# Performance work log

Measured on AMD Instinct MI355X. Metric: run time of the kernel, lower is better.

Reference implementation:

```python
import jax, jax.numpy as jnp
import numpy as np

D_MODEL = 512
D_INNER = 2 * D_MODEL          # Mamba expand=2
D_STATE = 16                   # Mamba default d_state
D_CONV = 4                     # Mamba default d_conv
DT_RANK = D_MODEL // 16        # ceil(512/16) = 32
B, L = 2, 2048


def setup_inputs() -> dict:
    key = jax.random.key(0)
    ks = jax.random.split(key, 12)
    s = 0.02
    return {
        "query": jax.random.normal(ks[0], (B, L, D_MODEL), jnp.float32),
        "value": jax.random.normal(ks[1], (B, L, D_MODEL), jnp.float32),
        "diff_ts": jax.random.normal(ks[2], (B, D_MODEL), jnp.float32),
        # AdaLN modulation: SiLU -> Linear(D, 2D) (random instead of zero-init to exercise math)
        "ada_w": jax.random.normal(ks[3], (2 * D_MODEL, D_MODEL), jnp.float32) * s,
        "ada_b": jax.random.normal(ks[4], (2 * D_MODEL,), jnp.float32) * s,
        # Mamba params
        "in_proj_w": jax.random.normal(ks[5], (2 * D_INNER, D_MODEL), jnp.float32) * s,
        "conv_w": jax.random.normal(ks[6], (D_INNER, D_CONV), jnp.float32) * 0.1,
        "conv_b": jax.random.normal(ks[7], (D_INNER,), jnp.float32) * 0.1,
        "x_proj_w": jax.random.normal(ks[8], (DT_RANK + 2 * D_STATE, D_INNER), jnp.float32) * s,
        "dt_proj_w": jax.random.normal(ks[9], (D_INNER, DT_RANK), jnp.float32) * 0.1,
        "dt_proj_b": jax.random.normal(ks[10], (D_INNER,), jnp.float32) * 0.1,
        "A_log": jnp.broadcast_to(jnp.log(jnp.arange(1, D_STATE + 1, dtype=jnp.float32)), (D_INNER, D_STATE)) * jnp.ones((D_INNER, 1), jnp.float32),
        "D_param": jnp.ones((D_INNER,), jnp.float32),
        "out_proj_w": jax.random.normal(ks[11], (D_MODEL, D_INNER), jnp.float32) * s,
        "ln_g": jnp.ones((D_MODEL,), jnp.float32),
        "ln_b": jnp.zeros((D_MODEL,), jnp.float32),
    }


def reference(query, value, diff_ts, ada_w, ada_b, in_proj_w, conv_w, conv_b,
              x_proj_w, dt_proj_w, dt_proj_b, A_log, D_param, out_proj_w, ln_g, ln_b):
    silu = jax.nn.silu
    # ---- AdaLN modulation of query ----
    m = silu(diff_ts) @ ada_w.T + ada_b            # (B, 2D)
    scale, shift = jnp.split(m, 2, axis=-1)        # (B, D) each
    x = query * (1.0 + scale[:, None, :]) + shift[:, None, :]

    # ---- Mamba block ----
    xz = x @ in_proj_w.T                           # (B, L, 2*d_inner)
    xm, z = jnp.split(xz, 2, axis=-1)
    # causal depthwise conv1d (kernel D_CONV)
    xp = jnp.pad(xm, ((0, 0), (D_CONV - 1, 0), (0, 0)))
    Lq = xm.shape[1]
    xc = sum(xp[:, k:k + Lq, :] * conv_w[:, k] for k in range(D_CONV)) + conv_b
    xc = silu(xc)                                  # (B, L, d_inner)

    xdb = xc @ x_proj_w.T                          # (B, L, dt_rank + 2*N)
    dt = xdb[..., :DT_RANK]
    Bm = xdb[..., DT_RANK:DT_RANK + D_STATE]       # (B, L, N)
    Cm = xdb[..., DT_RANK + D_STATE:]              # (B, L, N)
    delta = jax.nn.softplus(dt @ dt_proj_w.T + dt_proj_b)  # (B, L, d_inner)
    A = -jnp.exp(A_log)                            # (d_inner, N)

    # ---- selective scan: h_t = exp(dt*A) h_{t-1} + dt*B_t*x_t ; y_t = C_t . h_t ----
    def step(h, inp):
        d_t, x_t, B_t, C_t = inp                   # (B,d), (B,d), (B,N), (B,N)
        dA = jnp.exp(d_t[..., None] * A)           # (B, d, N)
        h = dA * h + (d_t * x_t)[..., None] * B_t[:, None, :]
        y = jnp.einsum('bdn,bn->bd', h, C_t)
        return h, y

    seq = (delta.transpose(1, 0, 2), xc.transpose(1, 0, 2),
           Bm.transpose(1, 0, 2), Cm.transpose(1, 0, 2))
    h0 = jnp.zeros((query.shape[0], D_INNER, D_STATE), delta.dtype)
    _, ys = jax.lax.scan(step, h0, seq)            # (L, B, d_inner)

    y = ys.transpose(1, 0, 2) + xc * D_param
    y = y * silu(z)
    attn = y @ out_proj_w.T                        # (B, L, D)

    # ---- residual (dropout p=0) + LayerNorm ----
    out = query + attn
    mu = out.mean(-1, keepdims=True)
    var = out.var(-1, keepdims=True)
    return (out - mu) / jnp.sqrt(var + 1e-5) * ln_g + ln_b
```

## Files before the change

### kernel.cpp

```cpp
#include <hip/hip_runtime.h>
#include <hip/hip_bf16.h>

#define D_MODEL 512
#define D_INNER 1024
#define D_STATE 16
#define DT_RANK 32
#define BB 2
#define LL 2048
#define RR (BB*LL)
#define NC 128
#define CS 16

typedef __attribute__((ext_vector_type(8))) short short8;
typedef __attribute__((ext_vector_type(4))) short short4v;
typedef __attribute__((ext_vector_type(4))) float f32x4;

static __device__ __forceinline__ short f2bf(float f) {
  union { __hip_bfloat16 h; short s; } u;
  u.h = __float2bfloat16(f);
  return u.s;
}

__global__ void k_ada_cvtw(const float* __restrict__ diff,
                           const float* __restrict__ aw,
                           const float* __restrict__ ab,
                           float* __restrict__ m,
                           const float* __restrict__ inw,
                           const float* __restrict__ outw,
                           short* __restrict__ inwb,
                           short* __restrict__ outwb) {
  const int bx = blockIdx.x;
  const int t = threadIdx.x;
  if (bx < 8) {
    __shared__ float sd[D_MODEL];
    const int b = bx >> 2;
    const int jb = bx & 3;
    for (int k = t; k < D_MODEL; k += 256) {
      float v = diff[b*D_MODEL + k];
      sd[k] = v / (1.f + __expf(-v));
    }
    __syncthreads();
    const int j = jb*256 + t;
    const float4* wr = reinterpret_cast<const float4*>(aw + (size_t)j*D_MODEL);
    float acc = ab[j];
    #pragma unroll 4
    for (int k4 = 0; k4 < D_MODEL/4; ++k4) {
      float4 wv = wr[k4];
      acc += sd[4*k4]*wv.x + sd[4*k4+1]*wv.y + sd[4*k4+2]*wv.z + sd[4*k4+3]*wv.w;
    }
    m[b*(2*D_MODEL) + j] = acc;
  } else {
    const int N1 = 2048*512, N2 = 512*1024;
    const int idx = ((bx - 8)*256 + t)*4;
    if (idx < N1) {
      float4 v = *reinterpret_cast<const float4*>(inw + idx);
      short4v s = {f2bf(v.x), f2bf(v.y), f2bf(v.z), f2bf(v.w)};
      *reinterpret_cast<short4v*>(inwb + idx) = s;
    } else if (idx < N1 + N2) {
      float4 v = *reinterpret_cast<const float4*>(outw + (idx - N1));
      short4v s = {f2bf(v.x), f2bf(v.y), f2bf(v.z), f2bf(v.w)};
      *reinterpret_cast<short4v*>(outwb + (idx - N1)) = s;
    }
  }
}

__global__ void k_amod(const float* __restrict__ q,
                       const float* __restrict__ m,
                       short* __restrict__ amod) {
  const int gid = blockIdx.x*256 + threadIdx.x;
  const int idx = gid*4;
  const int r = idx >> 9, k = idx & 511;
  const float* mrow = m + (r >> 11)*(2*D_MODEL);
  float4 a = *reinterpret_cast<const float4*>(q + idx);
  float4 s = *reinterpret_cast<const float4*>(mrow + k);
  float4 h = *reinterpret_cast<const float4*>(mrow + D_MODEL + k);
  short4v o = {f2bf(a.x*(1.f+s.x)+h.x), f2bf(a.y*(1.f+s.y)+h.y),
               f2bf(a.z*(1.f+s.z)+h.z), f2bf(a.w*(1.f+s.w)+h.w)};
  *reinterpret_cast<short4v*>(amod + idx) = o;
}

__global__ void __launch_bounds__(256) k_gemm_bf16(
    const short* __restrict__ A,
    const short* __restrict__ B,
    float* __restrict__ C,
    int K, int ldc) {
  __shared__ short As[128][48];
  __shared__ short Bs[64][48];
  const int t = threadIdx.x;
  const int wave = t >> 6, lane = t & 63;
  const int quad = lane >> 4, l16 = lane & 15;
  const int row0 = blockIdx.y*128;
  const int col0 = blockIdx.x*64;
  f32x4 acc[2][4] = {};
  for (int k0 = 0; k0 < K; k0 += 32) {
    #pragma unroll
    for (int i = 0; i < 2; ++i) {
      int e = t + i*256;
      int ar = e >> 2, ak = (e & 3)*8;
      *reinterpret_cast<short8*>(&As[ar][ak]) =
          *reinterpret_cast<const short8*>(A + (size_t)(row0+ar)*K + k0 + ak);
    }
    {
      int br = t >> 2, bk = (t & 3)*8;
      *reinterpret_cast<short8*>(&Bs[br][bk]) =
          *reinterpret_cast<const short8*>(B + (size_t)(col0+br)*K + k0 + bk);
    }
    __syncthreads();
    short8 af[2], bf[4];
    #pragma unroll
    for (int i = 0; i < 2; ++i)
      af[i] = *reinterpret_cast<const short8*>(&As[wave*32 + i*16 + l16][quad*8]);
    #pragma unroll
    for (int j = 0; j < 4; ++j)
      bf[j] = *reinterpret_cast<const short8*>(&Bs[j*16 + l16][quad*8]);
    #pragma unroll
    for (int i = 0; i < 2; ++i)
      #pragma unroll
      for (int j = 0; j < 4; ++j)
        acc[i][j] = __builtin_amdgcn_mfma_f32_16x16x32_bf16(af[i], bf[j], acc[i][j], 0, 0, 0);
    __syncthreads();
  }
  #pragma unroll
  for (int i = 0; i < 2; ++i)
    #pragma unroll
    for (int j = 0; j < 4; ++j)
      #pragma unroll
      for (int r = 0; r < 4; ++r)
        C[(size_t)(row0 + wave*32 + i*16 + quad*4 + r)*ldc + col0 + j*16 + l16] = acc[i][j][r];
}

__global__ void k_conv4(const float* __restrict__ xz,
                        const float* __restrict__ cw,
                        const float* __restrict__ cb,
                        float* __restrict__ xc) {
  const int gid = blockIdx.x*256 + threadIdx.x;
  const int d4 = (gid & 255)*4;
  const int r = gid >> 8;
  const int l = r & (LL-1);
  float4 w0 = *reinterpret_cast<const float4*>(cw + (size_t)(d4+0)*4);
  float4 w1 = *reinterpret_cast<const float4*>(cw + (size_t)(d4+1)*4);
  float4 w2 = *reinterpret_cast<const float4*>(cw + (size_t)(d4+2)*4);
  float4 w3 = *reinterpret_cast<const float4*>(cw + (size_t)(d4+3)*4);
  float4 res = *reinterpret_cast<const float4*>(cb + d4);
  #pragma unroll
  for (int k = 0; k < 4; ++k) {
    int ls = l + k - 3;
    if (ls >= 0) {
      float4 xv = *reinterpret_cast<const float4*>(xz + (size_t)(r + k - 3)*(2*D_INNER) + d4);
      float wk0 = (&w0.x)[k], wk1 = (&w1.x)[k], wk2 = (&w2.x)[k], wk3 = (&w3.x)[k];
      res.x += xv.x*wk0; res.y += xv.y*wk1; res.z += xv.z*wk2; res.w += xv.w*wk3;
    }
  }
  res.x = res.x / (1.f + __expf(-res.x));
  res.y = res.y / (1.f + __expf(-res.y));
  res.z = res.z / (1.f + __expf(-res.z));
  res.w = res.w / (1.f + __expf(-res.w));
  *reinterpret_cast<float4*>(xc + (size_t)r*D_INNER + d4) = res;
}

__global__ void k_xproj_t(const float* __restrict__ xc,
                          const float* __restrict__ xw,
                          float* __restrict__ xdb) {
  __shared__ float As[16][68];
  __shared__ float Bs[16][68];
  const int tx = threadIdx.x, ty = threadIdx.y;
  const int t = ty*16 + tx;
  const int row0 = blockIdx.y*64;
  const int kbase = blockIdx.x*128;
  float acc[4][4] = {};
  for (int k0 = kbase; k0 < kbase + 128; k0 += 16) {
    #pragma unroll
    for (int i = 0; i < 4; ++i) {
      int e = t + i*256;
      int kk = e & 15, rr = e >> 4;
      As[kk][rr] = xc[(size_t)(row0+rr)*D_INNER + k0+kk];
      Bs[kk][rr] = xw[(size_t)rr*D_INNER + k0+kk];
    }
    __syncthreads();
    #pragma unroll
    for (int kk = 0; kk < 16; ++kk) {
      float4 av = *reinterpret_cast<const float4*>(&As[kk][ty*4]);
      float4 bv = *reinterpret_cast<const float4*>(&Bs[kk][tx*4]);
      float a[4] = {av.x, av.y, av.z, av.w};
      float bq[4] = {bv.x, bv.y, bv.z, bv.w};
      #pragma unroll
      for (int i = 0; i < 4; ++i)
        #pragma unroll
        for (int j = 0; j < 4; ++j)
          acc[i][j] += a[i]*bq[j];
    }
    __syncthreads();
  }
  #pragma unroll
  for (int i = 0; i < 4; ++i)
    #pragma unroll
    for (int j = 0; j < 4; ++j)
      unsafeAtomicAdd(&xdb[(size_t)(row0+ty*4+i)*64 + tx*4 + j], acc[i][j]);
}

__global__ void __launch_bounds__(256) k_deltaf(
    const float* __restrict__ xdb,
    const float* __restrict__ dtw,
    const float* __restrict__ dtb,
    float* __restrict__ delta) {
  const int d = blockIdx.x*256 + threadIdx.x;
  const int r0 = blockIdx.y*16;
  float dwr[DT_RANK];
  const float4* dwp = reinterpret_cast<const float4*>(dtw + (size_t)d*DT_RANK);
  #pragma unroll
  for (int i = 0; i < 8; ++i) {
    float4 v = dwp[i];
    dwr[4*i]=v.x; dwr[4*i+1]=v.y; dwr[4*i+2]=v.z; dwr[4*i+3]=v.w;
  }
  const float dbv = dtb[d];
  for (int r = r0; r < r0 + 16; ++r) {
    const float4* xr = reinterpret_cast<const float4*>(xdb + (size_t)r*64);
    float acc = dbv;
    #pragma unroll
    for (int i = 0; i < 8; ++i) {
      float4 v = xr[i];
      acc += v.x*dwr[4*i] + v.y*dwr[4*i+1] + v.z*dwr[4*i+2] + v.w*dwr[4*i+3];
    }
    delta[(size_t)r*D_INNER + d] = (acc > 20.f) ? acc : __logf(1.f + __expf(acc));
  }
}


__global__ void __launch_bounds__(256) k_scan1(
    const float* __restrict__ delta,
    const float* __restrict__ xc,
    const float* __restrict__ xdb,
    float* __restrict__ rbuf,
    float* __restrict__ hstate) {
  __shared__ float sx[CS*64];
  const int tid = threadIdx.x;
  const int d = blockIdx.x*256 + tid;
  const int c = blockIdx.y;
  const int b = blockIdx.z;
  const float* xrow = xdb + ((size_t)b*LL + (size_t)c*CS)*64;
  *reinterpret_cast<float4*>(&sx[tid*4]) = *reinterpret_cast<const float4*>(xrow + tid*4);
  const size_t base = ((size_t)b*LL + (size_t)c*CS)*D_INNER + d;
  float dls[CS], xvs[CS];
  #pragma unroll
  for (int t = 0; t < CS; ++t) {
    dls[t] = delta[base + (size_t)t*D_INNER];
    xvs[t] = xc[base + (size_t)t*D_INNER];
  }
  float h[D_STATE];
  #pragma unroll
  for (int n = 0; n < D_STATE; ++n) h[n] = 0.f;
  float S = 0.f;
  __syncthreads();
  #pragma unroll
  for (int t = 0; t < CS; ++t) {
    float dlt = dls[t];
    S += dlt;
    float dx = dlt * xvs[t];
    float r = __expf(-dlt);
    float e = r;
    #pragma unroll
    for (int n = 0; n < D_STATE; ++n) {
      h[n] = e*h[n] + dx*sx[t*64 + 32 + n];
      e *= r;
    }
  }
  const size_t s0 = (((size_t)b*NC + c)*D_STATE)*D_INNER + d;
  #pragma unroll
  for (int n = 0; n < D_STATE; ++n)
    hstate[s0 + (size_t)n*D_INNER] = h[n];
  rbuf[((size_t)b*NC + c)*D_INNER + d] = __expf(-S);
}

__global__ void k_scan2(const float* __restrict__ rbuf,
                        float* __restrict__ hstate) {
  const int gid = blockIdx.x*256 + threadIdx.x;
  const int b = gid >> 14;
  const int nd = gid & 16383;
  const int n = nd >> 10;
  const int d = nd & (D_INNER-1);
  const int p = n + 1;
  float h = 0.f;
  #pragma unroll 4
  for (int c = 0; c < NC; ++c) {
    const size_t ridx = ((size_t)b*NC + c)*D_INNER + d;
    const size_t idx = (((size_t)b*NC + c)*D_STATE)*D_INNER + nd;
    float r = rbuf[ridx];
    float hl = hstate[idx];
    float r2 = r*r, r4 = r2*r2, r8 = r4*r4;
    float a = (p & 1) ? r : 1.f;
    if (p & 2)  a *= r2;
    if (p & 4)  a *= r4;
    if (p & 8)  a *= r8;
    if (p & 16) a *= r8*r8;
    hstate[idx] = h;
    h = a*h + hl;
  }
}

__global__ void __launch_bounds__(256) k_scan3(
    const float* __restrict__ delta,
    const float* __restrict__ xc,
    const float* __restrict__ xdb,
    const float* __restrict__ hstate,
    const float* __restrict__ Dp,
    const float* __restrict__ xz,
    short* __restrict__ y2b) {
  __shared__ float sx[CS*64];
  const int tid = threadIdx.x;
  const int d = blockIdx.x*256 + tid;
  const int c = blockIdx.y;
  const int b = blockIdx.z;
  const float* xrow = xdb + ((size_t)b*LL + (size_t)c*CS)*64;
  *reinterpret_cast<float4*>(&sx[tid*4]) = *reinterpret_cast<const float4*>(xrow + tid*4);
  const size_t r0 = (size_t)b*LL + (size_t)c*CS;
  const size_t base = r0*D_INNER + d;
  float dls[CS], xvs[CS], zs[CS];
  #pragma unroll
  for (int t = 0; t < CS; ++t) {
    dls[t] = delta[base + (size_t)t*D_INNER];
    xvs[t] = xc[base + (size_t)t*D_INNER];
    zs[t]  = xz[(r0 + t)*(2*D_INNER) + D_INNER + d];
  }
  float h[D_STATE];
  const size_t s0 = (((size_t)b*NC + c)*D_STATE)*D_INNER + d;
  #pragma unroll
  for (int n = 0; n < D_STATE; ++n)
    h[n] = hstate[s0 + (size_t)n*D_INNER];
  const float dp = Dp[d];
  __syncthreads();
  #pragma unroll
  for (int t = 0; t < CS; ++t) {
    float dlt = dls[t];
    float xv  = xvs[t];
    float dx = dlt * xv;
    float r = __expf(-dlt);
    float e = r;
    float acc = 0.f;
    #pragma unroll
    for (int n = 0; n < D_STATE; ++n) {
      h[n] = e*h[n] + dx*sx[t*64 + 32 + n];
      acc += h[n]*sx[t*64 + 48 + n];
      e *= r;
    }
    float z = zs[t];
    float sz = z / (1.f + __expf(-z));
    y2b[base + (size_t)t*D_INNER] = f2bf((acc + xv*dp) * sz);
  }
}

__global__ void k_ln(const float* __restrict__ attn,
                     const float* __restrict__ q,
                     const float* __restrict__ g,
                     const float* __restrict__ bb,
                     float* __restrict__ out) {
  const int r = blockIdx.x;
  const int t = threadIdx.x;
  float v0 = attn[(size_t)r*D_MODEL + t]       + q[(size_t)r*D_MODEL + t];
  float v1 = attn[(size_t)r*D_MODEL + 256 + t] + q[(size_t)r*D_MODEL + 256 + t];
  float s = v0 + v1, sq = v0*v0 + v1*v1;
  #pragma unroll
  for (int off = 32; off; off >>= 1) {
    s  += __shfl_xor(s, off);
    sq += __shfl_xor(sq, off);
  }
  __shared__ float ss[4], qq[4], stats[2];
  const int wid = t >> 6, lane = t & 63;
  if (lane == 0) { ss[wid] = s; qq[wid] = sq; }
  __syncthreads();
  if (t == 0) {
    float S = ss[0]+ss[1]+ss[2]+ss[3];
    float Q = qq[0]+qq[1]+qq[2]+qq[3];
    float mu = S * (1.f/D_MODEL);
    float var = Q * (1.f/D_MODEL) - mu*mu;
    stats[0] = mu; stats[1] = rsqrtf(var + 1e-5f);
  }
  __syncthreads();
  float mu = stats[0], rs = stats[1];
  out[(size_t)r*D_MODEL + t]       = (v0-mu)*rs*g[t]     + bb[t];
  out[(size_t)r*D_MODEL + 256 + t] = (v1-mu)*rs*g[256+t] + bb[256+t];
}

extern "C" void kernel_launch(void* const* d_in, const int* in_sizes, int n_in,
                              void* d_out, int out_size, void* d_ws, size_t ws_size,
                              hipStream_t stream) {
  (void)in_sizes; (void)n_in; (void)out_size; (void)ws_size;
  const float* q    = (const float*)d_in[0];
  const float* diff = (const float*)d_in[2];
  const float* aw   = (const float*)d_in[3];
  const float* ab   = (const float*)d_in[4];
  const float* inw  = (const float*)d_in[5];
  const float* cw   = (const float*)d_in[6];
  const float* cb   = (const float*)d_in[7];
  const float* xw   = (const float*)d_in[8];
  const float* dtw  = (const float*)d_in[9];
  const float* dtb  = (const float*)d_in[10];
  const float* Dp   = (const float*)d_in[12];
  const float* outw = (const float*)d_in[13];
  const float* lng  = (const float*)d_in[14];
  const float* lnb  = (const float*)d_in[15];
  float* out = (float*)d_out;

  float* ws = (float*)d_ws;
  float* m      = ws;
  float* xz     = ws + 2048;
  float* xc     = xz + (size_t)RR*2*D_INNER;
  float* xdb    = xc + (size_t)RR*D_INNER;
  float* rbuf   = xdb + (size_t)RR*64;
  float* hstate = rbuf + (size_t)BB*NC*D_INNER;
  float* delta  = hstate + (size_t)BB*NC*D_INNER*16;
  float* attn2  = delta + (size_t)RR*D_INNER;
  short* amod  = (short*)(attn2 + (size_t)RR*D_MODEL);
  short* inwb  = amod + (size_t)RR*D_MODEL;
  short* outwb = inwb + (size_t)2*D_INNER*D_MODEL;
  short* y2b   = outwb + (size_t)D_MODEL*D_INNER;

  k_ada_cvtw<<<8 + (2048*512 + 512*1024)/(256*4), 256, 0, stream>>>(
      diff, aw, ab, m, inw, outw, inwb, outwb);
  k_amod<<<(RR*D_MODEL)/(256*4), 256, 0, stream>>>(q, m, amod);
  k_gemm_bf16<<<dim3((2*D_INNER)/64, RR/128), 256, 0, stream>>>(amod, inwb, xz, D_MODEL, 2*D_INNER);
  k_conv4<<<(RR*D_INNER/4)/256, 256, 0, stream>>>(xz, cw, cb, xc);
  hipMemsetAsync(xdb, 0, (size_t)RR*64*sizeof(float), stream);
  k_xproj_t<<<dim3(8, RR/64), dim3(16,16), 0, stream>>>(xc, xw, xdb);
  k_deltaf<<<dim3(D_INNER/256, RR/16), 256, 0, stream>>>(xdb, dtw, dtb, delta);
  k_scan1<<<dim3(D_INNER/256, NC, BB), 256, 0, stream>>>(delta, xc, xdb, rbuf, hstate);
  k_scan2<<<(BB*D_INNER*16)/256, 256, 0, stream>>>(rbuf, hstate);
  k_scan3<<<dim3(D_INNER/256, NC, BB), 256, 0, stream>>>(delta, xc, xdb, hstate, Dp, xz, y2b);
  k_gemm_bf16<<<dim3(D_MODEL/64, RR/128), 256, 0, stream>>>(y2b, outwb, attn2, D_INNER, D_MODEL);
  k_ln<<<RR, 256, 0, stream>>>(attn2, q, lng, lnb, out);
}
```

Baseline: 281.8 us.

## Fuse delta computation into scan kernels and run x_proj as bf16 MFMA GEMM

```diff
diff --git a/kernel.cpp b/kernel.cpp
--- a/kernel.cpp
+++ b/kernel.cpp
@@ -27,8 +27,10 @@
                            float* __restrict__ m,
                            const float* __restrict__ inw,
                            const float* __restrict__ outw,
+                           const float* __restrict__ xw,
                            short* __restrict__ inwb,
-                           short* __restrict__ outwb) {
+                           short* __restrict__ outwb,
+                           short* __restrict__ xwb) {
   const int bx = blockIdx.x;
   const int t = threadIdx.x;
   if (bx < 8) {
@@ -50,7 +52,7 @@
     }
     m[b*(2*D_MODEL) + j] = acc;
   } else {
-    const int N1 = 2048*512, N2 = 512*1024;
+    const int N1 = 2048*512, N2 = 512*1024, N3 = 64*1024;
     const int idx = ((bx - 8)*256 + t)*4;
     if (idx < N1) {
       float4 v = *reinterpret_cast<const float4*>(inw + idx);
@@ -60,6 +62,10 @@
       float4 v = *reinterpret_cast<const float4*>(outw + (idx - N1));
       short4v s = {f2bf(v.x), f2bf(v.y), f2bf(v.z), f2bf(v.w)};
       *reinterpret_cast<short4v*>(outwb + (idx - N1)) = s;
+    } else if (idx < N1 + N2 + N3) {
+      float4 v = *reinterpret_cast<const float4*>(xw + (idx - N1 - N2));
+      short4v s = {f2bf(v.x), f2bf(v.y), f2bf(v.z), f2bf(v.w)};
+      *reinterpret_cast<short4v*>(xwb + (idx - N1 - N2)) = s;
     }
   }
 }
@@ -132,7 +138,8 @@
 __global__ void k_conv4(const float* __restrict__ xz,
                         const float* __restrict__ cw,
                         const float* __restrict__ cb,
-                        float* __restrict__ xc) {
+                        float* __restrict__ xc,
+                        short* __restrict__ xcb) {
   const int gid = blockIdx.x*256 + threadIdx.x;
   const int d4 = (gid & 255)*4;
   const int r = gid >> 8;
@@ -156,80 +163,16 @@
   res.z = res.z / (1.f + __expf(-res.z));
   res.w = res.w / (1.f + __expf(-res.w));
   *reinterpret_cast<float4*>(xc + (size_t)r*D_INNER + d4) = res;
-}
-
-__global__ void k_xproj_t(const float* __restrict__ xc,
-                          const float* __restrict__ xw,
-                          float* __restrict__ xdb) {
-  __shared__ float As[16][68];
-  __shared__ float Bs[16][68];
-  const int tx = threadIdx.x, ty = threadIdx.y;
-  const int t = ty*16 + tx;
-  const int row0 = blockIdx.y*64;
-  const int kbase = blockIdx.x*128;
-  float acc[4][4] = {};
-  for (int k0 = kbase; k0 < kbase + 128; k0 += 16) {
-    #pragma unroll
-    for (int i = 0; i < 4; ++i) {
-      int e = t + i*256;
-      int kk = e & 15, rr = e >> 4;
-      As[kk][rr] = xc[(size_t)(row0+rr)*D_INNER + k0+kk];
-      Bs[kk][rr] = xw[(size_t)rr*D_INNER + k0+kk];
-    }
-    __syncthreads();
-    #pragma unroll
-    for (int kk = 0; kk < 16; ++kk) {
-      float4 av = *reinterpret_cast<const float4*>(&As[kk][ty*4]);
-      float4 bv = *reinterpret_cast<const float4*>(&Bs[kk][tx*4]);
-      float a[4] = {av.x, av.y, av.z, av.w};
-      float bq[4] = {bv.x, bv.y, bv.z, bv.w};
-      #pragma unroll
-      for (int i = 0; i < 4; ++i)
-        #pragma unroll
-        for (int j = 0; j < 4; ++j)
-          acc[i][j] += a[i]*bq[j];
-    }
-    __syncthreads();
-  }
-  #pragma unroll
-  for (int i = 0; i < 4; ++i)
-    #pragma unroll
-    for (int j = 0; j < 4; ++j)
-      unsafeAtomicAdd(&xdb[(size_t)(row0+ty*4+i)*64 + tx*4 + j], acc[i][j]);
-}
-
-__global__ void __launch_bounds__(256) k_deltaf(
+  short4v rb = {f2bf(res.x), f2bf(res.y), f2bf(res.z), f2bf(res.w)};
+  *reinterpret_cast<short4v*>(xcb + (size_t)r*D_INNER + d4) = rb;
+}
+
+
+__global__ void __launch_bounds__(256) k_scan1(
+    const float* __restrict__ xc,
     const float* __restrict__ xdb,
     const float* __restrict__ dtw,
     const float* __restrict__ dtb,
-    float* __restrict__ delta) {
-  const int d = blockIdx.x*256 + threadIdx.x;
-  const int r0 = blockIdx.y*16;
-  float dwr[DT_RANK];
-  const float4* dwp = reinterpret_cast<const float4*>(dtw + (size_t)d*DT_RANK);
-  #pragma unroll
-  for (int i = 0; i < 8; ++i) {
-    float4 v = dwp[i];
-    dwr[4*i]=v.x; dwr[4*i+1]=v.y; dwr[4*i+2]=v.z; dwr[4*i+3]=v.w;
-  }
-  const float dbv = dtb[d];
-  for (int r = r0; r < r0 + 16; ++r) {
-    const float4* xr = reinterpret_cast<const float4*>(xdb + (size_t)r*64);
-    float acc = dbv;
-    #pragma unroll
-    for (int i = 0; i < 8; ++i) {
-      float4 v = xr[i];
-      acc += v.x*dwr[4*i] + v.y*dwr[4*i+1] + v.z*dwr[4*i+2] + v.w*dwr[4*i+3];
-    }
-    delta[(size_t)r*D_INNER + d] = (acc > 20.f) ? acc : __logf(1.f + __expf(acc));
-  }
-}
-
-
-__global__ void __launch_bounds__(256) k_scan1(
-    const float* __restrict__ delta,
-    const float* __restrict__ xc,
-    const float* __restrict__ xdb,
     float* __restrict__ rbuf,
     float* __restrict__ hstate) {
   __shared__ float sx[CS*64];
@@ -240,23 +183,34 @@
   const float* xrow = xdb + ((size_t)b*LL + (size_t)c*CS)*64;
   *reinterpret_cast<float4*>(&sx[tid*4]) = *reinterpret_cast<const float4*>(xrow + tid*4);
   const size_t base = ((size_t)b*LL + (size_t)c*CS)*D_INNER + d;
-  float dls[CS], xvs[CS];
+  float xvs[CS];
+  #pragma unroll
+  for (int t = 0; t < CS; ++t)
+    xvs[t] = xc[base + (size_t)t*D_INNER];
+  float dwr[DT_RANK];
+  const float4* dwp = reinterpret_cast<const float4*>(dtw + (size_t)d*DT_RANK);
+  #pragma unroll
+  for (int i = 0; i < 8; ++i) {
+    float4 v = dwp[i];
+    dwr[4*i]=v.x; dwr[4*i+1]=v.y; dwr[4*i+2]=v.z; dwr[4*i+3]=v.w;
+  }
+  const float dbv = dtb[d];
+  float h[D_STATE];
+  #pragma unroll
+  for (int n = 0; n < D_STATE; ++n) h[n] = 0.f;
+  float rtot = 1.f;
+  __syncthreads();
   #pragma unroll
   for (int t = 0; t < CS; ++t) {
-    dls[t] = delta[base + (size_t)t*D_INNER];
-    xvs[t] = xc[base + (size_t)t*D_INNER];
-  }
-  float h[D_STATE];
-  #pragma unroll
-  for (int n = 0; n < D_STATE; ++n) h[n] = 0.f;
-  float S = 0.f;
-  __syncthreads();
-  #pragma unroll
-  for (int t = 0; t < CS; ++t) {
-    float dlt = dls[t];
-    S += dlt;
+    float dacc = dbv;
+    #pragma unroll
+    for (int i = 0; i < DT_RANK; ++i)
+      dacc += sx[t*64 + i]*dwr[i];
+    float ex = __expf(dacc);
+    float dlt = (dacc > 20.f) ? dacc : __logf(1.f + ex);
+    float r = 1.f / (1.f + ex);
+    rtot *= r;
     float dx = dlt * xvs[t];
-    float r = __expf(-dlt);
     float e = r;
     #pragma unroll
     for (int n = 0; n < D_STATE; ++n) {
@@ -268,7 +222,7 @@
   #pragma unroll
   for (int n = 0; n < D_STATE; ++n)
     hstate[s0 + (size_t)n*D_INNER] = h[n];
-  rbuf[((size_t)b*NC + c)*D_INNER + d] = __expf(-S);
+  rbuf[((size_t)b*NC + c)*D_INNER + d] = rtot;
 }
 
 __global__ void k_scan2(const float* __restrict__ rbuf,
@@ -298,9 +252,10 @@
 }
 
 __global__ void __launch_bounds__(256) k_scan3(
-    const float* __restrict__ delta,
     const float* __restrict__ xc,
     const float* __restrict__ xdb,
+    const float* __restrict__ dtw,
+    const float* __restrict__ dtb,
     const float* __restrict__ hstate,
     const float* __restrict__ Dp,
     const float* __restrict__ xz,
@@ -314,13 +269,20 @@
   *reinterpret_cast<float4*>(&sx[tid*4]) = *reinterpret_cast<const float4*>(xrow + tid*4);
   const size_t r0 = (size_t)b*LL + (size_t)c*CS;
   const size_t base = r0*D_INNER + d;
-  float dls[CS], xvs[CS], zs[CS];
+  float xvs[CS], zs[CS];
   #pragma unroll
   for (int t = 0; t < CS; ++t) {
-    dls[t] = delta[base + (size_t)t*D_INNER];
     xvs[t] = xc[base + (size_t)t*D_INNER];
     zs[t]  = xz[(r0 + t)*(2*D_INNER) + D_INNER + d];
   }
+  float dwr[DT_RANK];
+  const float4* dwp = reinterpret_cast<const float4*>(dtw + (size_t)d*DT_RANK);
+  #pragma unroll
+  for (int i = 0; i < 8; ++i) {
+    float4 v = dwp[i];
+    dwr[4*i]=v.x; dwr[4*i+1]=v.y; dwr[4*i+2]=v.z; dwr[4*i+3]=v.w;
+  }
+  const float dbv = dtb[d];
   float h[D_STATE];
   const size_t s0 = (((size_t)b*NC + c)*D_STATE)*D_INNER + d;
   #pragma unroll
@@ -330,10 +292,15 @@
   __syncthreads();
   #pragma unroll
   for (int t = 0; t < CS; ++t) {
-    float dlt = dls[t];
-    float xv  = xvs[t];
+    float dacc = dbv;
+    #pragma unroll
+    for (int i = 0; i < DT_RANK; ++i)
+      dacc += sx[t*64 + i]*dwr[i];
+    float ex = __expf(dacc);
+    float dlt = (dacc > 20.f) ? dacc : __logf(1.f + ex);
+    float r = 1.f / (1.f + ex);
+    float xv = xvs[t];
     float dx = dlt * xv;
-    float r = __expf(-dlt);
     float e = r;
     float acc = 0.f;
     #pragma unroll
@@ -407,24 +374,24 @@
   float* xdb    = xc + (size_t)RR*D_INNER;
   float* rbuf   = xdb + (size_t)RR*64;
   float* hstate = rbuf + (size_t)BB*NC*D_INNER;
-  float* delta  = hstate + (size_t)BB*NC*D_INNER*16;
-  float* attn2  = delta + (size_t)RR*D_INNER;
+  float* attn2  = hstate + (size_t)BB*NC*D_INNER*16;
   short* amod  = (short*)(attn2 + (size_t)RR*D_MODEL);
   short* inwb  = amod + (size_t)RR*D_MODEL;
   short* outwb = inwb + (size_t)2*D_INNER*D_MODEL;
-  short* y2b   = outwb + (size_t)D_MODEL*D_INNER;
-
-  k_ada_cvtw<<<8 + (2048*512 + 512*1024)/(256*4), 256, 0, stream>>>(
-      diff, aw, ab, m, inw, outw, inwb, outwb);
+  short* xwb   = outwb + (size_t)D_MODEL*D_INNER;
+  short* y2b   = xwb + (size_t)64*D_INNER;
+  short* xcb   = y2b + (size_t)RR*D_INNER;
+
+  const int cvtBlocks = (2048*512 + 512*1024 + 64*1024)/(256*4);
+  k_ada_cvtw<<<8 + cvtBlocks, 256, 0, stream>>>(
+      diff, aw, ab, m, inw, outw, xw, inwb, outwb, xwb);
   k_amod<<<(RR*D_MODEL)/(256*4), 256, 0, stream>>>(q, m, amod);
   k_gemm_bf16<<<dim3((2*D_INNER)/64, RR/128), 256, 0, stream>>>(amod, inwb, xz, D_MODEL, 2*D_INNER);
-  k_conv4<<<(RR*D_INNER/4)/256, 256, 0, stream>>>(xz, cw, cb, xc);
-  hipMemsetAsync(xdb, 0, (size_t)RR*64*sizeof(float), stream);
-  k_xproj_t<<<dim3(8, RR/64), dim3(16,16), 0, stream>>>(xc, xw, xdb);
-  k_deltaf<<<dim3(D_INNER/256, RR/16), 256, 0, stream>>>(xdb, dtw, dtb, delta);
-  k_scan1<<<dim3(D_INNER/256, NC, BB), 256, 0, stream>>>(delta, xc, xdb, rbuf, hstate);
+  k_conv4<<<(RR*D_INNER/4)/256, 256, 0, stream>>>(xz, cw, cb, xc, xcb);
+  k_gemm_bf16<<<dim3(1, RR/128), 256, 0, stream>>>(xcb, xwb, xdb, D_INNER, 64);
+  k_scan1<<<dim3(D_INNER/256, NC, BB), 256, 0, stream>>>(xc, xdb, dtw, dtb, rbuf, hstate);
   k_scan2<<<(BB*D_INNER*16)/256, 256, 0, stream>>>(rbuf, hstate);
-  k_scan3<<<dim3(D_INNER/256, NC, BB), 256, 0, stream>>>(delta, xc, xdb, hstate, Dp, xz, y2b);
+  k_scan3<<<dim3(D_INNER/256, NC, BB), 256, 0, stream>>>(xc, xdb, dtw, dtb, hstate, Dp, xz, y2b);
   k_gemm_bf16<<<dim3(D_MODEL/64, RR/128), 256, 0, stream>>>(y2b, outwb, attn2, D_INNER, D_MODEL);
   k_ln<<<RR, 256, 0, stream>>>(attn2, q, lng, lnb, out);
 }
```

After: 263.8 us. 6.4% less time.
